# Optimization experiments

Hardware: AMD Instinct MI355X
Metric: run time of the kernel (lower is better)

## Reference

```python
import jax, jax.numpy as jnp
import numpy as np

# dims: batch, seq, d_model, heads, experts, expert hidden, top-k
B, S, D, H, E, F, K = 8, 512, 768, 12, 8, 3072, 2
DH = D // H
TAU = 1.0  # routing temperature
EPS = 1e-5


def _ln(x, g, b):
    mu = jnp.mean(x, axis=-1, keepdims=True)
    var = jnp.var(x, axis=-1, keepdims=True)
    return (x - mu) * jax.lax.rsqrt(var + EPS) * g + b


def setup_inputs() -> dict:
    key = jax.random.key(0)
    ks = jax.random.split(key, 12)
    sd = 1.0 / np.sqrt(D)
    sf = 1.0 / np.sqrt(F)
    return {
        "x": jax.random.normal(ks[0], (B, S, D), jnp.float32),
        "wq": jax.random.normal(ks[1], (D, D), jnp.float32) * sd,
        "wk": jax.random.normal(ks[2], (D, D), jnp.float32) * sd,
        "wv": jax.random.normal(ks[3], (D, D), jnp.float32) * sd,
        "wo": jax.random.normal(ks[4], (D, D), jnp.float32) * sd,
        "ln1_g": jnp.ones((D,), jnp.float32),
        "ln1_b": jnp.zeros((D,), jnp.float32),
        "ln2_g": jnp.ones((D,), jnp.float32),
        "ln2_b": jnp.zeros((D,), jnp.float32),
        "gate_w": jax.random.normal(ks[5], (D, E), jnp.float32) * sd,
        "gate_b": jnp.zeros((E,), jnp.float32),
        "bias_e": jnp.zeros((E,), jnp.float32),  # bias_param: per-expert routing bias (selection only)
        "w1": jax.random.normal(ks[6], (E, D, F), jnp.float32) * sd,
        "b1": jnp.zeros((E, F), jnp.float32),
        "w2": jax.random.normal(ks[7], (E, F, D), jnp.float32) * sf,
        "b2": jnp.zeros((E, D), jnp.float32),
    }


def reference(x, wq, wk, wv, wo, ln1_g, ln1_b, ln2_g, ln2_b,
              gate_w, gate_b, bias_e, w1, b1, w2, b2):
    # --- pre-LN multi-head self-attention + residual ---
    h = _ln(x, ln1_g, ln1_b)
    q = (h @ wq).reshape(B, S, H, DH)
    k = (h @ wk).reshape(B, S, H, DH)
    v = (h @ wv).reshape(B, S, H, DH)
    scores = jnp.einsum("bqhd,bkhd->bhqk", q, k) / np.sqrt(DH).astype(np.float32)
    attn = jax.nn.softmax(scores, axis=-1)
    o = jnp.einsum("bhqk,bkhd->bqhd", attn, v).reshape(B, S, D) @ wo
    x = x + o

    # --- pre-LN top-k MoE + residual ---
    h = _ln(x, ln2_g, ln2_b).reshape(B * S, D)          # [T, D]
    logits = (h @ gate_w + gate_b) / TAU                # [T, E]
    sel_scores = logits + bias_e                        # bias used for selection only
    _, idx = jax.lax.top_k(sel_scores, K)               # [T, K]
    topk_logits = jnp.take_along_axis(logits, idx, axis=-1)
    gates = jax.nn.softmax(topk_logits, axis=-1)        # [T, K]
    # sparse combine weights [T, E]
    cw = jnp.zeros((B * S, E), x.dtype).at[jnp.arange(B * S)[:, None], idx].set(gates)
    mid = jax.nn.gelu(jnp.einsum("td,edf->tef", h, w1) + b1)   # [T, E, F]
    eout = jnp.einsum("tef,efd->ted", mid, w2) + b2            # [T, E, D]
    y = jnp.einsum("ted,te->td", eout, cw).reshape(B, S, D)
    return x + y
```

## Files before the change

### kernel.cpp

```cpp
#include <hip/hip_runtime.h>
#include <hip/hip_bf16.h>

using bf16 = __hip_bfloat16;

constexpr int NB = 8, NS = 512, ND = 768, NH = 12, NE = 8, NF = 3072, NT = 4096;
constexpr int HG = 4;
constexpr int NG = NH / HG;
constexpr int GW = HG * 64;
constexpr int FQ = 768;
constexpr int NP = NF / FQ;
constexpr int CS = 32;

typedef __attribute__((ext_vector_type(8))) short v8s;
typedef __attribute__((ext_vector_type(4))) float v4f;

__device__ __forceinline__ short f2bf(float v) {
    bf16 t = __float2bfloat16(v);
    return *reinterpret_cast<short*>(&t);
}
__device__ __forceinline__ float bf2f(short s) {
    bf16 t = *reinterpret_cast<bf16*>(&s);
    return __bfloat162float(t);
}

__launch_bounds__(256)
__global__ void ln_kernel(const float* __restrict__ x, const float* __restrict__ g,
                          const float* __restrict__ b, float* __restrict__ out) {
    const int t = blockIdx.x;
    const int tid = threadIdx.x;
    const float* xr = x + (size_t)t * ND;
    float v0 = xr[tid], v1 = xr[tid + 256], v2 = xr[tid + 512];
    float s = v0 + v1 + v2;
    float ss = v0 * v0 + v1 * v1 + v2 * v2;
#pragma unroll
    for (int off = 32; off >= 1; off >>= 1) {
        s += __shfl_xor(s, off);
        ss += __shfl_xor(ss, off);
    }
    __shared__ float rs[4], rss[4];
    const int wv = tid >> 6, ln = tid & 63;
    if (ln == 0) { rs[wv] = s; rss[wv] = ss; }
    __syncthreads();
    float S = rs[0] + rs[1] + rs[2] + rs[3];
    float SS = rss[0] + rss[1] + rss[2] + rss[3];
    float mu = S * (1.0f / ND);
    float var = SS * (1.0f / ND) - mu * mu;
    float r = rsqrtf(fmaxf(var, 0.f) + 1e-5f);
    float* orow = out + (size_t)t * ND;
    orow[tid]       = (v0 - mu) * r * g[tid]       + b[tid];
    orow[tid + 256] = (v1 - mu) * r * g[tid + 256] + b[tid + 256];
    orow[tid + 512] = (v2 - mu) * r * g[tid + 512] + b[tid + 512];
}

__device__ __forceinline__ void gemm3_core(const float* __restrict__ A, int lda,
                                           const float* __restrict__ Bsrc, int ldb,
                                           int Kd, int m0, v4f acc[4],
                                           short* Ah, short* Al, short* Bh, short* Bl) {
    const int tid = threadIdx.x, lane = tid & 63, wv = tid >> 6;
    const int qd = lane >> 4, l16 = lane & 15;
    const int ar = tid >> 2, ac = (tid & 3) * 8;
    const int bn = tid & 63, bk = (tid >> 6) * 8;
    const float* Arow = A + (size_t)(m0 + ar) * lda;
    for (int k0 = 0; k0 < Kd; k0 += 32) {
        {
            const float* asrc = Arow + k0 + ac;
            v8s ah, al;
#pragma unroll
            for (int j = 0; j < 8; j++) {
                float vv = asrc[j];
                short hi = f2bf(vv);
                ah[j] = hi;
                al[j] = f2bf(vv - bf2f(hi));
            }
            *(v8s*)&Ah[ar * 40 + ac] = ah;
            *(v8s*)&Al[ar * 40 + ac] = al;
        }
        {
            const float* bsrc = Bsrc + (size_t)(k0 + bk) * ldb + bn;
            v8s bh_, bl_;
#pragma unroll
            for (int j = 0; j < 8; j++) {
                float vv = bsrc[(size_t)j * ldb];
                short hi = f2bf(vv);
                bh_[j] = hi;
                bl_[j] = f2bf(vv - bf2f(hi));
            }
            *(v8s*)&Bh[bn * 40 + bk] = bh_;
            *(v8s*)&Bl[bn * 40 + bk] = bl_;
        }
        __syncthreads();
        v8s bhf = *(const v8s*)&Bh[(wv * 16 + l16) * 40 + qd * 8];
        v8s blf = *(const v8s*)&Bl[(wv * 16 + l16) * 40 + qd * 8];
#pragma unroll
        for (int t = 0; t < 4; t++) {
            v8s ahf = *(const v8s*)&Ah[(t * 16 + l16) * 40 + qd * 8];
            v8s alf = *(const v8s*)&Al[(t * 16 + l16) * 40 + qd * 8];
            acc[t] = __builtin_amdgcn_mfma_f32_16x16x32_bf16(ahf, bhf, acc[t], 0, 0, 0);
            acc[t] = __builtin_amdgcn_mfma_f32_16x16x32_bf16(ahf, blf, acc[t], 0, 0, 0);
            acc[t] = __builtin_amdgcn_mfma_f32_16x16x32_bf16(alf, bhf, acc[t], 0, 0, 0);
        }
        __syncthreads();
    }
}

template <int RES_MODE>
__launch_bounds__(256)
__global__ void sgemm3(const float* __restrict__ A, int lda, const float* __restrict__ Bw,
                       int ldb, int bcol0, const float* __restrict__ Res,
                       float* __restrict__ C, int ldc, int Kd) {
    __shared__ short Ah[64 * 40], Al[64 * 40], Bh[64 * 40], Bl[64 * 40];
    const int m0 = blockIdx.x * 64, n0 = blockIdx.y * 64;
    v4f acc[4] = {};
    gemm3_core(A, lda, Bw + bcol0 + n0, ldb, Kd, m0, acc, Ah, Al, Bh, Bl);
    const int tid = threadIdx.x, lane = tid & 63, wv = tid >> 6;
    const int qd = lane >> 4, l16 = lane & 15;
    const int c = n0 + wv * 16 + l16;
#pragma unroll
    for (int t = 0; t < 4; t++)
#pragma unroll
        for (int rg = 0; rg < 4; rg++) {
            const int r = m0 + t * 16 + qd * 4 + rg;
            size_t ci = (size_t)r * ldc + c;
            if (RES_MODE == 0) C[ci] = acc[t][rg];
            else if (RES_MODE == 1) C[ci] = Res[ci] + acc[t][rg];
            else C[ci] += acc[t][rg];
        }
}

__launch_bounds__(256)
__global__ void qkv3(const float* __restrict__ h, const float* __restrict__ wq,
                     const float* __restrict__ wk, const float* __restrict__ wv,
                     int bcol0, float* __restrict__ qo, float* __restrict__ ko,
                     float* __restrict__ vo) {
    __shared__ short Ah[64 * 40], Al[64 * 40], Bh[64 * 40], Bl[64 * 40];
    const int m0 = blockIdx.x * 64;
    const int ysel = blockIdx.y >> 2, ny = blockIdx.y & 3;
    const int n0 = ny * 64;
    const float* Bw = (ysel == 0) ? wq : (ysel == 1) ? wk : wv;
    float* C = (ysel == 0) ? qo : (ysel == 1) ? ko : vo;
    v4f acc[4] = {};
    gemm3_core(h, ND, Bw + bcol0 + n0, ND, ND, m0, acc, Ah, Al, Bh, Bl);
    const int tid = threadIdx.x, lane = tid & 63, wv_ = tid >> 6;
    const int qd = lane >> 4, l16 = lane & 15;
    const int c = n0 + wv_ * 16 + l16;
#pragma unroll
    for (int t = 0; t < 4; t++)
#pragma unroll
        for (int rg = 0; rg < 4; rg++) {
            const int r = m0 + t * 16 + qd * 4 + rg;
            C[(size_t)r * GW + c] = acc[t][rg];
        }
}

__launch_bounds__(512)
__global__ void attn_kernel(const float* __restrict__ q, const float* __restrict__ k,
                            const float* __restrict__ v, float* __restrict__ o) {
    __shared__ float qs[32][68];
    __shared__ float kp[64][68];
    __shared__ float vs[64][68];
    const int qt = blockIdx.x, hl = blockIdx.y, b = blockIdx.z;
    const int tid = threadIdx.x;
    const int tx = tid & 15, rw = tid >> 4;
    const int hc = hl * 64;
    {
        const v4f* q4 = (const v4f*)(q + ((size_t)b * NS + qt * 32) * GW + hc);
        *(v4f*)&qs[rw][tx * 4] = q4[(size_t)rw * (GW / 4) + tx];
    }
    float oa[4] = {};
    float mi = -1.0e30f, li = 0.f;
    for (int kt = 0; kt < NS / 64; kt++) {
        __syncthreads();
        {
            const v4f* k4 = (const v4f*)(k + ((size_t)b * NS + kt * 64) * GW + hc);
            const v4f* v4 = (const v4f*)(v + ((size_t)b * NS + kt * 64) * GW + hc);
#pragma unroll
            for (int i = 0; i < 2; i++) {
                int idx = tid + 512 * i;
                int r = idx >> 4, c4 = idx & 15;
                *(v4f*)&kp[r][c4 * 4] = k4[(size_t)r * (GW / 4) + c4];
                *(v4f*)&vs[r][c4 * 4] = v4[(size_t)r * (GW / 4) + c4];
            }
        }
        __syncthreads();
        float s[4] = {};
#pragma unroll
        for (int d0 = 0; d0 < 64; d0 += 4) {
            v4f av = *(const v4f*)&qs[rw][d0];
            v4f bv[4];
#pragma unroll
            for (int j = 0; j < 4; j++) bv[j] = *(const v4f*)&kp[tx + 16 * j][d0];
#pragma unroll
            for (int dd = 0; dd < 4; dd++)
#pragma unroll
                for (int j = 0; j < 4; j++) s[j] += av[dd] * bv[j][dd];
        }
#pragma unroll
        for (int j = 0; j < 4; j++) s[j] *= 0.125f;
        float mt = fmaxf(fmaxf(s[0], s[1]), fmaxf(s[2], s[3]));
#pragma unroll
        for (int off = 1; off < 16; off <<= 1) mt = fmaxf(mt, __shfl_xor(mt, off));
        float mn = fmaxf(mi, mt);
        float al = __expf(mi - mn);
        mi = mn;
        float rsum = 0.f;
#pragma unroll
        for (int j = 0; j < 4; j++) {
            s[j] = __expf(s[j] - mn);
            rsum += s[j];
        }
#pragma unroll
        for (int off = 1; off < 16; off <<= 1) rsum += __shfl_xor(rsum, off);
        li = li * al + rsum;
        __syncthreads();
#pragma unroll
        for (int j = 0; j < 4; j++) {
            kp[rw][tx + 16 * j] = s[j];
            oa[j] *= al;
        }
        __syncthreads();
#pragma unroll
        for (int d0 = 0; d0 < 64; d0 += 4) {
            v4f av = *(const v4f*)&kp[rw][d0];
#pragma unroll
            for (int dd = 0; dd < 4; dd++) {
                float bb[4];
#pragma unroll
                for (int j = 0; j < 4; j++) bb[j] = vs[d0 + dd][tx + 16 * j];
#pragma unroll
                for (int j = 0; j < 4; j++) oa[j] += av[dd] * bb[j];
            }
        }
    }
    float inv = 1.0f / li;
#pragma unroll
    for (int j = 0; j < 4; j++)
        o[((size_t)b * NS + qt * 32 + rw) * GW + hc + tx + 16 * j] = oa[j] * inv;
}

__launch_bounds__(256)
__global__ void route_kernel(const float* __restrict__ x1, const float* __restrict__ lg,
                             const float* __restrict__ lb, const float* __restrict__ gw,
                             const float* __restrict__ gb, const float* __restrict__ be,
                             int* __restrict__ cnt, int* __restrict__ list,
                             float* __restrict__ gates, bf16* __restrict__ h2) {
    __shared__ int se[8], sent[8];
    const int lane = threadIdx.x & 63;
    const int wv = threadIdx.x >> 6;
    const int t = blockIdx.x * 4 + wv;
    const float* xr = x1 + (size_t)t * ND;
    float xv[12];
    float s = 0.f, ss = 0.f;
#pragma unroll
    for (int i = 0; i < 12; i++) {
        xv[i] = xr[i * 64 + lane];
        s += xv[i];
        ss += xv[i] * xv[i];
    }
#pragma unroll
    for (int off = 32; off >= 1; off >>= 1) {
        s += __shfl_xor(s, off);
        ss += __shfl_xor(ss, off);
    }
    float mu = s * (1.0f / ND);
    float var = ss * (1.0f / ND) - mu * mu;
    float r = rsqrtf(fmaxf(var, 0.f) + 1e-5f);
    float le[NE];
#pragma unroll
    for (int e = 0; e < NE; e++) le[e] = 0.f;
    bf16* h2r = h2 + (size_t)t * ND;
#pragma unroll
    for (int i = 0; i < 12; i++) {
        int d = i * 64 + lane;
        float hn = (xv[i] - mu) * r * lg[d] + lb[d];
        h2r[d] = __float2bfloat16(hn);
#pragma unroll
        for (int e = 0; e < NE; e++) le[e] += hn * gw[d * NE + e];
    }
#pragma unroll
    for (int off = 1; off < 64; off <<= 1)
#pragma unroll
        for (int e = 0; e < NE; e++) le[e] += __shfl_xor(le[e], off);
    float m1 = -1.0e30f, m2 = -1.0e30f, l1 = 0.f, l2 = 0.f;
    int i1 = 0, i2 = 0;
#pragma unroll
    for (int e = 0; e < NE; e++) {
        float lv = le[e] + gb[e];
        float sv = lv + be[e];
        bool g1 = sv > m1;
        float pm1 = m1, pl1 = l1; int pi1 = i1;
        m1 = g1 ? sv : m1; l1 = g1 ? lv : l1; i1 = g1 ? e : i1;
        bool g2 = (!g1) && (sv > m2);
        m2 = g1 ? pm1 : (g2 ? sv : m2);
        l2 = g1 ? pl1 : (g2 ? lv : l2);
        i2 = g1 ? pi1 : (g2 ? e : i2);
    }
    float m = fmaxf(l1, l2);
    float e1 = __expf(l1 - m), e2 = __expf(l2 - m);
    float inv = 1.0f / (e1 + e2);
    if (lane == 0) {
        gates[t * 2 + 0] = e1 * inv;
        gates[t * 2 + 1] = e2 * inv;
        se[wv * 2]       = i1; sent[wv * 2]       = t * 2;
        se[wv * 2 + 1]   = i2; sent[wv * 2 + 1]   = t * 2 + 1;
    }
    __syncthreads();
    if (threadIdx.x < NE) {
        const int e = threadIdx.x;
        int c = 0;
#pragma unroll
        for (int sl = 0; sl < 8; sl++) c += (se[sl] == e) ? 1 : 0;
        if (c) {
            int p = atomicAdd(&cnt[e * CS], c);
#pragma unroll
            for (int sl = 0; sl < 8; sl++)
                if (se[sl] == e) {
                    if (p < NT) list[e * NT + p] = sent[sl];
                    p++;
                }
        }
    }
}

__launch_bounds__(256)
__global__ void moe_gemm1(const bf16* __restrict__ h2, const float* __restrict__ w1,
                          const float* __restrict__ b1, const int* __restrict__ cnt,
                          const int* __restrict__ list, bf16* __restrict__ mid, int fcol0) {
    const int e = blockIdx.x >> 6, tile = blockIdx.x & 63;
    const int n = min(cnt[e * CS], NT);
    const int r0 = tile * 64;
    if (r0 >= n) return;
    const int f0 = blockIdx.y * 64;
    __shared__ int ent[64];
    __shared__ short As[64 * 40];
    __shared__ short Bs[64 * 40];
    const int tid = threadIdx.x;
    const int lane = tid & 63, wv = tid >> 6;
    const int qd = lane >> 4, l16 = lane & 15;
    if (tid < 64) {
        int en = (r0 + tid < n) ? list[e * NT + r0 + tid] : -1;
        if (en < 0 || en >= 2 * NT) en = -1;
        ent[tid] = en;
    }
    __syncthreads();
    v4f acc[4] = {};
    const float* w1e = w1 + (size_t)e * ND * NF + fcol0 + f0;
    const int ar = tid >> 2, ac = (tid & 3) * 8;
    const int bn = tid & 63, bk = (tid >> 6) * 8;
    const int aen = ent[ar];
    for (int k0 = 0; k0 < ND; k0 += 32) {
        v8s av = {};
        if (aen >= 0)
            av = *(const v8s*)((const short*)h2 + (size_t)(aen >> 1) * ND + k0 + ac);
        *(v8s*)&As[ar * 40 + ac] = av;
        {
            const float* src = w1e + (size_t)(k0 + bk) * NF + bn;
            v8s bv;
#pragma unroll
            for (int j = 0; j < 8; j++) bv[j] = f2bf(src[(size_t)j * NF]);
            *(v8s*)&Bs[bn * 40 + bk] = bv;
        }
        __syncthreads();
        v8s bfrag = *(const v8s*)&Bs[(wv * 16 + l16) * 40 + qd * 8];
#pragma unroll
        for (int t = 0; t < 4; t++) {
            v8s afrag = *(const v8s*)&As[(t * 16 + l16) * 40 + qd * 8];
            acc[t] = __builtin_amdgcn_mfma_f32_16x16x32_bf16(afrag, bfrag, acc[t], 0, 0, 0);
        }
        __syncthreads();
    }
    const int col = wv * 16 + l16;
    const float bias = b1[e * NF + fcol0 + f0 + col];
#pragma unroll
    for (int t = 0; t < 4; t++) {
#pragma unroll
        for (int rg = 0; rg < 4; rg++) {
            int en = ent[t * 16 + qd * 4 + rg];
            if (en < 0) continue;
            float xv = acc[t][rg] + bias;
            float th = tanhf(0.7978845608028654f * (xv + 0.044715f * xv * xv * xv));
            mid[((size_t)((en & 1) * NT) + (en >> 1)) * FQ + f0 + col] =
                __float2bfloat16(0.5f * xv * (1.0f + th));
        }
    }
}

__launch_bounds__(256)
__global__ void moe_gemm2(const bf16* __restrict__ mid, const float* __restrict__ w2,
                          const float* __restrict__ b2, const int* __restrict__ cnt,
                          const int* __restrict__ list, const float* __restrict__ gates,
                          float* __restrict__ x1, int fcol0, int add_b2) {
    const int e = blockIdx.x >> 6, tile = blockIdx.x & 63;
    const int n = min(cnt[e * CS], NT);
    const int r0 = tile * 64;
    if (r0 >= n) return;
    const int d0 = blockIdx.y * 64;
    __shared__ int ent[64];
    __shared__ short As[64 * 40];
    __shared__ short Bs[64 * 40];
    const int tid = threadIdx.x;
    const int lane = tid & 63, wv = tid >> 6;
    const int qd = lane >> 4, l16 = lane & 15;
    if (tid < 64) {
        int en = (r0 + tid < n) ? list[e * NT + r0 + tid] : -1;
        if (en < 0 || en >= 2 * NT) en = -1;
        ent[tid] = en;
    }
    __syncthreads();
    v4f acc[4] = {};
    const float* w2e = w2 + (size_t)e * NF * ND + d0;
    const int ar = tid >> 2, ac = (tid & 3) * 8;
    const int bn = tid & 63, bk = (tid >> 6) * 8;
    const int aen = ent[ar];
    for (int k0 = 0; k0 < FQ; k0 += 32) {
        v8s av = {};
        if (aen >= 0)
            av = *(const v8s*)((const short*)mid +
                               ((size_t)((aen & 1) * NT) + (aen >> 1)) * FQ + k0 + ac);
        *(v8s*)&As[ar * 40 + ac] = av;
        {
            const float* src = w2e + (size_t)(fcol0 + k0 + bk) * ND + bn;
            v8s bv;
#pragma unroll
            for (int j = 0; j < 8; j++) bv[j] = f2bf(src[(size_t)j * ND]);
            *(v8s*)&Bs[bn * 40 + bk] = bv;
        }
        __syncthreads();
        v8s bfrag = *(const v8s*)&Bs[(wv * 16 + l16) * 40 + qd * 8];
#pragma unroll
        for (int t = 0; t < 4; t++) {
            v8s afrag = *(const v8s*)&As[(t * 16 + l16) * 40 + qd * 8];
            acc[t] = __builtin_amdgcn_mfma_f32_16x16x32_bf16(afrag, bfrag, acc[t], 0, 0, 0);
        }
        __syncthreads();
    }
    const int col = wv * 16 + l16;
    const float bias = add_b2 ? b2[e * ND + d0 + col] : 0.f;
#pragma unroll
    for (int t = 0; t < 4; t++) {
#pragma unroll
        for (int rg = 0; rg < 4; rg++) {
            int en = ent[t * 16 + qd * 4 + rg];
            if (en < 0) continue;
            float g = gates[en];
            atomicAdd(&x1[(size_t)(en >> 1) * ND + d0 + col], g * (acc[t][rg] + bias));
        }
    }
}

__launch_bounds__(256)
__global__ void final_kernel(const float* __restrict__ x1, float* __restrict__ out) {
    int i = blockIdx.x * 256 + threadIdx.x;
    out[i] = x1[i];
}

extern "C" void kernel_launch(void* const* d_in, const int* in_sizes, int n_in,
                              void* d_out, int out_size, void* d_ws, size_t ws_size,
                              hipStream_t stream) {
    const float* x    = (const float*)d_in[0];
    const float* wq   = (const float*)d_in[1];
    const float* wk   = (const float*)d_in[2];
    const float* wvp  = (const float*)d_in[3];
    const float* wo   = (const float*)d_in[4];
    const float* ln1g = (const float*)d_in[5];
    const float* ln1b = (const float*)d_in[6];
    const float* ln2g = (const float*)d_in[7];
    const float* ln2b = (const float*)d_in[8];
    const float* gw   = (const float*)d_in[9];
    const float* gb   = (const float*)d_in[10];
    const float* be   = (const float*)d_in[11];
    const float* w1   = (const float*)d_in[12];
    const float* b1   = (const float*)d_in[13];
    const float* w2   = (const float*)d_in[14];
    const float* b2   = (const float*)d_in[15];
    float* out = (float*)d_out;

    const size_t TDn = (size_t)NT * ND;
    const size_t TGn = (size_t)NT * GW;
    float* W = (float*)d_ws;
    int*   cnt   = (int*)W;
    int*   list  = cnt + NE * CS;
    float* gates = (float*)(list + NE * NT);
    float* x1 = W + 41216;
    float* h  = x1 + TDn;
    float* R0 = h + TDn;
    float* q  = R0;
    float* k  = R0 + TGn;
    float* v  = R0 + 2 * TGn;
    float* og = R0 + 3 * TGn;
    bf16*  h2  = (bf16*)h;
    bf16*  mid = (bf16*)R0;

    hipMemsetAsync(cnt, 0, NE * CS * sizeof(int), stream);

    ln_kernel<<<NT, 256, 0, stream>>>(x, ln1g, ln1b, h);
    for (int g = 0; g < NG; g++) {
        qkv3<<<dim3(NT / 64, 12), 256, 0, stream>>>(h, wq, wk, wvp, g * GW, q, k, v);
        attn_kernel<<<dim3(NS / 32, HG, NB), 512, 0, stream>>>(q, k, v, og);
        if (g == 0)
            sgemm3<1><<<dim3(NT / 64, ND / 64), 256, 0, stream>>>(
                og, GW, wo + (size_t)g * GW * ND, ND, 0, x, x1, ND, GW);
        else
            sgemm3<2><<<dim3(NT / 64, ND / 64), 256, 0, stream>>>(
                og, GW, wo + (size_t)g * GW * ND, ND, 0, nullptr, x1, ND, GW);
    }
    route_kernel<<<NT / 4, 256, 0, stream>>>(x1, ln2g, ln2b, gw, gb, be, cnt, list,
                                             gates, h2);
    for (int p = 0; p < NP; p++) {
        int fcol0 = p * FQ;
        moe_gemm1<<<dim3(NE * (NT / 64), FQ / 64), 256, 0, stream>>>(
            h2, w1, b1, cnt, list, mid, fcol0);
        moe_gemm2<<<dim3(NE * (NT / 64), ND / 64), 256, 0, stream>>>(
            mid, w2, b2, cnt, list, gates, x1, fcol0, p == 0 ? 1 : 0);
    }
    final_kernel<<<TDn / 256, 256, 0, stream>>>(x1, out);
}
```

Baseline: 1.164 ms.

## Pre-convert and transpose MoE expert weights to bf16 before each GEMM

Adds a cvt_w kernel that, for each F-chunk, transposes the fp32 w1/w2 slices through shared memory and stores them as k-contiguous bf16. The MoE GEMMs then load B fragments straight from global memory with one vector load per lane, instead of each tile block re-reading strided fp32 weights, converting them and staging them in LDS. This removes the redundant per-tile conversion and the strided fp32 traffic, and frees the Bs shared buffer. The cost is extra conversion launches and a workspace round trip every chunk, plus buffer aliasing changes (h2 and mid swap regions) that must not overlap the new weight buffer.

Measured after the change: 1.163 ms. About the same (-0.1%).

```diff
diff --git a/kernel.cpp b/kernel.cpp
--- a/kernel.cpp
+++ b/kernel.cpp
@@ -322,7 +322,40 @@
 }
 
 __launch_bounds__(256)
-__global__ void moe_gemm1(const bf16* __restrict__ h2, const float* __restrict__ w1,
+__global__ void cvt_w(const float* __restrict__ src, size_t eStride, int rowStride,
+                      int rowOff, int colOff, short* __restrict__ dst) {
+    __shared__ float tile[64][65];
+    const int bx = blockIdx.x, by = blockIdx.y, e = blockIdx.z;
+    const int tid = threadIdx.x;
+    {
+        const int c4 = (tid & 15) * 4, r = tid >> 4;
+        const float* sp = src + (size_t)e * eStride +
+                          (size_t)(rowOff + by * 64 + r) * rowStride + colOff + bx * 64 + c4;
+#pragma unroll
+        for (int i = 0; i < 4; i++) {
+            v4f vv = *(const v4f*)(sp + (size_t)(16 * i) * rowStride);
+            tile[r + 16 * i][c4] = vv[0]; tile[r + 16 * i][c4 + 1] = vv[1];
+            tile[r + 16 * i][c4 + 2] = vv[2]; tile[r + 16 * i][c4 + 3] = vv[3];
+        }
+    }
+    __syncthreads();
+    {
+        const int lc = tid >> 2;
+        const int lr0 = (tid & 3) * 16;
+        short* d = dst + ((size_t)e * 768 + bx * 64 + lc) * 768 + by * 64 + lr0;
+        v8s o0, o1;
+#pragma unroll
+        for (int j = 0; j < 8; j++) {
+            o0[j] = f2bf(tile[lr0 + j][lc]);
+            o1[j] = f2bf(tile[lr0 + 8 + j][lc]);
+        }
+        *(v8s*)d = o0;
+        *(v8s*)&d[8] = o1;
+    }
+}
+
+__launch_bounds__(256)
+__global__ void moe_gemm1(const bf16* __restrict__ h2, const short* __restrict__ wt,
                           const float* __restrict__ b1, const int* __restrict__ cnt,
                           const int* __restrict__ list, bf16* __restrict__ mid, int fcol0) {
     const int e = blockIdx.x >> 6, tile = blockIdx.x & 63;
@@ -332,7 +365,6 @@
     const int f0 = blockIdx.y * 64;
     __shared__ int ent[64];
     __shared__ short As[64 * 40];
-    __shared__ short Bs[64 * 40];
     const int tid = threadIdx.x;
     const int lane = tid & 63, wv = tid >> 6;
     const int qd = lane >> 4, l16 = lane & 15;
@@ -343,24 +375,16 @@
     }
     __syncthreads();
     v4f acc[4] = {};
-    const float* w1e = w1 + (size_t)e * ND * NF + fcol0 + f0;
+    const short* wfr = wt + ((size_t)e * 768 + f0 + wv * 16 + l16) * 768 + qd * 8;
     const int ar = tid >> 2, ac = (tid & 3) * 8;
-    const int bn = tid & 63, bk = (tid >> 6) * 8;
     const int aen = ent[ar];
+    const short* arow = (const short*)h2 + (size_t)(aen >= 0 ? (aen >> 1) : 0) * ND + ac;
     for (int k0 = 0; k0 < ND; k0 += 32) {
         v8s av = {};
-        if (aen >= 0)
-            av = *(const v8s*)((const short*)h2 + (size_t)(aen >> 1) * ND + k0 + ac);
+        if (aen >= 0) av = *(const v8s*)(arow + k0);
         *(v8s*)&As[ar * 40 + ac] = av;
-        {
-            const float* src = w1e + (size_t)(k0 + bk) * NF + bn;
-            v8s bv;
-#pragma unroll
-            for (int j = 0; j < 8; j++) bv[j] = f2bf(src[(size_t)j * NF]);
-            *(v8s*)&Bs[bn * 40 + bk] = bv;
-        }
-        __syncthreads();
-        v8s bfrag = *(const v8s*)&Bs[(wv * 16 + l16) * 40 + qd * 8];
+        v8s bfrag = *(const v8s*)(wfr + k0);
+        __syncthreads();
 #pragma unroll
         for (int t = 0; t < 4; t++) {
             v8s afrag = *(const v8s*)&As[(t * 16 + l16) * 40 + qd * 8];
@@ -385,7 +409,7 @@
 }
 
 __launch_bounds__(256)
-__global__ void moe_gemm2(const bf16* __restrict__ mid, const float* __restrict__ w2,
+__global__ void moe_gemm2(const bf16* __restrict__ mid, const short* __restrict__ wt,
                           const float* __restrict__ b2, const int* __restrict__ cnt,
                           const int* __restrict__ list, const float* __restrict__ gates,
                           float* __restrict__ x1, int fcol0, int add_b2) {
@@ -396,7 +420,6 @@
     const int d0 = blockIdx.y * 64;
     __shared__ int ent[64];
     __shared__ short As[64 * 40];
-    __shared__ short Bs[64 * 40];
     const int tid = threadIdx.x;
     const int lane = tid & 63, wv = tid >> 6;
     const int qd = lane >> 4, l16 = lane & 15;
@@ -407,25 +430,17 @@
     }
     __syncthreads();
     v4f acc[4] = {};
-    const float* w2e = w2 + (size_t)e * NF * ND + d0;
+    const short* wfr = wt + ((size_t)e * 768 + d0 + wv * 16 + l16) * 768 + qd * 8;
     const int ar = tid >> 2, ac = (tid & 3) * 8;
-    const int bn = tid & 63, bk = (tid >> 6) * 8;
     const int aen = ent[ar];
+    const short* arow = (const short*)mid +
+                        ((size_t)(aen >= 0 ? ((aen & 1) * NT + (aen >> 1)) : 0)) * FQ + ac;
     for (int k0 = 0; k0 < FQ; k0 += 32) {
         v8s av = {};
-        if (aen >= 0)
-            av = *(const v8s*)((const short*)mid +
-                               ((size_t)((aen & 1) * NT) + (aen >> 1)) * FQ + k0 + ac);
+        if (aen >= 0) av = *(const v8s*)(arow + k0);
         *(v8s*)&As[ar * 40 + ac] = av;
-        {
-            const float* src = w2e + (size_t)(fcol0 + k0 + bk) * ND + bn;
-            v8s bv;
-#pragma unroll
-            for (int j = 0; j < 8; j++) bv[j] = f2bf(src[(size_t)j * ND]);
-            *(v8s*)&Bs[bn * 40 + bk] = bv;
-        }
-        __syncthreads();
-        v8s bfrag = *(const v8s*)&Bs[(wv * 16 + l16) * 40 + qd * 8];
+        v8s bfrag = *(const v8s*)(wfr + k0);
+        __syncthreads();
 #pragma unroll
         for (int t = 0; t < 4; t++) {
             v8s afrag = *(const v8s*)&As[(t * 16 + l16) * 40 + qd * 8];
@@ -487,8 +502,9 @@
     float* k  = R0 + TGn;
     float* v  = R0 + 2 * TGn;
     float* og = R0 + 3 * TGn;
-    bf16*  h2  = (bf16*)h;
-    bf16*  mid = (bf16*)R0;
+    bf16*  h2  = (bf16*)R0;
+    short* wt  = (short*)(R0 + TDn / 2);
+    bf16*  mid = (bf16*)h;
 
     hipMemsetAsync(cnt, 0, NE * CS * sizeof(int), stream);
 
@@ -507,10 +523,12 @@
                                              gates, h2);
     for (int p = 0; p < NP; p++) {
         int fcol0 = p * FQ;
+        cvt_w<<<dim3(12, 12, NE), 256, 0, stream>>>(w1, (size_t)ND * NF, NF, 0, fcol0, wt);
         moe_gemm1<<<dim3(NE * (NT / 64), FQ / 64), 256, 0, stream>>>(
-            h2, w1, b1, cnt, list, mid, fcol0);
+            h2, wt, b1, cnt, list, mid, fcol0);
+        cvt_w<<<dim3(12, 12, NE), 256, 0, stream>>>(w2, (size_t)NF * ND, ND, fcol0, 0, wt);
         moe_gemm2<<<dim3(NE * (NT / 64), ND / 64), 256, 0, stream>>>(
-            mid, w2, b2, cnt, list, gates, x1, fcol0, p == 0 ? 1 : 0);
+            mid, wt, b2, cnt, list, gates, x1, fcol0, p == 0 ? 1 : 0);
     }
     final_kernel<<<TDn / 256, 256, 0, stream>>>(x1, out);
 }
```
